# Kernel tuning notes

Hardware: AMD Instinct MI355X
Metric: run time of the kernel (lower is better)

The kernel has to match this reference:

```python
import jax, jax.numpy as jnp
import numpy as np

B = 512        # batch size
NCLASS = 128   # number of classes == embedding dim (per module docstring)
K = 8          # topk hard mining
MARGIN = 1.0
P = 1.0 / NCLASS  # default p = 1/nclass


def _pairwise_distances(x):
    # Euclidean distance matrix, with the zero-distance sqrt-safety trick
    dot = x @ x.T                      # (B, B)
    sq = jnp.diag(dot)                 # (B,)
    d = sq[None, :] - 2.0 * dot + sq[:, None]
    d = jnp.maximum(d, 0.0)
    zmask = (d == 0.0).astype(x.dtype)
    return (1.0 - zmask) * jnp.sqrt(d + zmask * 1e-16)


def _topk_rows_mask(valid):
    # torch .topk(k, dim=0, largest=True) + scatter_(0, idx, True):
    # per column, mark the k rows with the largest values.
    _, idx = jax.lax.top_k(valid.T, K)                 # (B, K): row indices per column
    mT = jnp.zeros((B, B), dtype=bool).at[jnp.arange(B)[:, None], idx].set(True)
    return mT.T                                        # back to (row, col) layout


def _forward(x, target):
    d = _pairwise_distances(x)                         # (B, B)
    sim = target[None, :] == target[:, None]           # (B, B) same-class mask

    # hard positives: largest same-class distances per column
    hard_pos = _topk_rows_mask(jnp.where(sim, d, -jnp.inf)) & sim
    # hard negatives: smallest different-class distances per column
    hard_neg = _topk_rows_mask(-jnp.where(sim, jnp.inf, d)) & (~sim)

    # minor-class anchors: class count < int(p * batch)
    boundary = int(P * B)
    cnt = jnp.zeros((NCLASS,), dtype=jnp.int32).at[target].add(1)
    anchors = cnt[target] < boundary                   # (B,)

    eye = jnp.eye(B, dtype=bool)
    mask_ap = (~eye) & anchors[:, None] & hard_pos     # (B, B)
    mask_an = anchors[:, None] & hard_neg              # (B, B)

    # O(B^3) triplet tensor
    t = d[:, :, None] - d[:, None, :] + MARGIN         # (B, B, B)
    m = mask_ap[:, :, None] & mask_an[:, None, :]
    t = jnp.maximum(m.astype(x.dtype) * t, 0.0)
    num_pos = jnp.sum(t > 1e-7).astype(x.dtype)
    return jnp.sum(t) / (num_pos + 1e-7)


def setup_inputs() -> dict:
    key = jax.random.key(0)
    k1, k2 = jax.random.split(key)
    x = jax.random.normal(k1, (B, NCLASS), dtype=jnp.float32)
    target = jax.random.randint(k2, (B,), 0, NCLASS)
    return {"x": x, "target": target}


def reference(x, target):
    return _forward(x, target)
```

## Files before the change

kernel.cpp:

```cpp
#include <hip/hip_runtime.h>
#include <math.h>

#define BB 512
#define DD 128
#define KK 8
#define BOUNDARY 4


__global__ __launch_bounds__(256) void fused_kernel(
    const float* __restrict__ x, const int* __restrict__ tgt,
    float* __restrict__ partS, int* __restrict__ partC)
{
    __shared__ float4 xi4[DD / 4];
    __shared__ float s_vn[BB];
    __shared__ float s_sq[BB];
    __shared__ int   s_tgt[BB];
    __shared__ int   s_cnt[128];
    __shared__ int   s_sel[KK];
    __shared__ int   s_pr[16], s_pj[16];
    __shared__ int   s_np;

    int k = blockIdx.x;
    int t = threadIdx.x;
    if (t < DD / 4) xi4[t] = ((const float4*)(x + k * DD))[t];
    if (t < 128) s_cnt[t] = 0;
    if (t == 0) s_np = 0;
    s_tgt[t]       = tgt[t];
    s_tgt[t + 256] = tgt[t + 256];
    __syncthreads();
    int tk = s_tgt[k];

    float q0 = 0.f, q1 = 0.f, q2 = 0.f, q3 = 0.f;
    for (int c = 0; c < DD / 4; ++c) {
        float4 a = xi4[c];
        q0 += a.x * a.x; q1 += a.y * a.y; q2 += a.z * a.z; q3 += a.w * a.w;
    }
    float sqk = (q0 + q1) + (q2 + q3);

    {
        int g = t >> 3, sub = t & 7;
        for (int pass = 0; pass < 16; ++pass) {
            int r = pass * 32 + g;
            const float4* xr = (const float4*)(x + r * DD);
            float d0 = 0.f, d1 = 0.f, d2 = 0.f, d3 = 0.f;
            float s0 = 0.f, s1 = 0.f, s2 = 0.f, s3 = 0.f;
            {
                float4 a = xi4[sub],      b = xr[sub];
                d0 = a.x*b.x + a.y*b.y + a.z*b.z + a.w*b.w;
                s0 = b.x*b.x + b.y*b.y + b.z*b.z + b.w*b.w;
            }
            {
                float4 a = xi4[sub + 8],  b = xr[sub + 8];
                d1 = a.x*b.x + a.y*b.y + a.z*b.z + a.w*b.w;
                s1 = b.x*b.x + b.y*b.y + b.z*b.z + b.w*b.w;
            }
            {
                float4 a = xi4[sub + 16], b = xr[sub + 16];
                d2 = a.x*b.x + a.y*b.y + a.z*b.z + a.w*b.w;
                s2 = b.x*b.x + b.y*b.y + b.z*b.z + b.w*b.w;
            }
            {
                float4 a = xi4[sub + 24], b = xr[sub + 24];
                d3 = a.x*b.x + a.y*b.y + a.z*b.z + a.w*b.w;
                s3 = b.x*b.x + b.y*b.y + b.z*b.z + b.w*b.w;
            }
            float dot = (d0 + d1) + (d2 + d3);
            float sq  = (s0 + s1) + (s2 + s3);
            for (int off = 4; off > 0; off >>= 1) {
                dot += __shfl_down(dot, off, 8);
                sq  += __shfl_down(sq,  off, 8);
            }
            if (sub == 0) {
                float dsq = fmaxf((sqk + sq) - 2.f * dot, 0.f);
                float dv = (dsq == 0.f) ? 0.f : sqrtf(dsq);
                s_sq[r] = sq;
                s_vn[r] = (s_tgt[r] == tk) ? -INFINITY : -dv;
            }
        }
    }
    __syncthreads();

    int wave = t >> 6, lane = t & 63;
    if (wave == 0) {
        float v[8];
        for (int q = 0; q < 8; ++q) v[q] = s_vn[q * 64 + lane];
        for (int pass = 0; pass < KK; ++pass) {
            float bv = -INFINITY; int bq = -1;
            for (int q = 0; q < 8; ++q)
                if (v[q] > bv) { bv = v[q]; bq = q; }
            int bi = (bq >= 0) ? (bq * 64 + lane) : (1 << 30);
            for (int off = 32; off > 0; off >>= 1) {
                float ov = __shfl_down(bv, off);
                int   oi = __shfl_down(bi, off);
                if (ov > bv || (ov == bv && oi < bi)) { bv = ov; bi = oi; }
            }
            bv = __shfl(bv, 0); bi = __shfl(bi, 0);
            if (lane == 0) s_sel[pass] = (bv == -INFINITY) ? -1 : bi;
            if ((bi & 63) == lane) v[bi >> 6] = -INFINITY;
        }
    } else if (wave == 1) {
        for (int q = 0; q < 8; ++q) atomicAdd(&s_cnt[s_tgt[q * 64 + lane]], 1);
    }
    __syncthreads();

    {
        int p = t >> 5, l = t & 31;
        int r = s_sel[p];
        if (r >= 0) {
            int tr = s_tgt[r];
            if (s_cnt[tr] < BOUNDARY) {
                for (int j = l; j < BB; j += 32)
                    if (j != r && s_tgt[j] == tr) {
                        int idx = atomicAdd(&s_np, 1);
                        s_pr[idx] = r; s_pj[idx] = j;
                    }
            }
        }
    }
    __syncthreads();

    float s = 0.f; int c = 0;
    if (t < s_np) {
        int r = s_pr[t], j = s_pj[t];
        const float4* xr = (const float4*)(x + r * DD);
        const float4* xj = (const float4*)(x + j * DD);
        float d0 = 0.f, d1 = 0.f, d2 = 0.f, d3 = 0.f;
        for (int cc = 0; cc < DD / 4; ++cc) {
            float4 a = xr[cc], b = xj[cc];
            d0 += a.x * b.x; d1 += a.y * b.y; d2 += a.z * b.z; d3 += a.w * b.w;
        }
        float dot = (d0 + d1) + (d2 + d3);
        float dsq = fmaxf((s_sq[r] + s_sq[j]) - 2.f * dot, 0.f);
        float dpos = (dsq == 0.f) ? 0.f : sqrtf(dsq);
        float tv = dpos + s_vn[r] + 1.0f;
        if (tv > 0.f) { s = tv; c = (tv > 1e-7f) ? 1 : 0; }
    }
    if (wave == 0) {
        for (int off = 32; off > 0; off >>= 1) {
            s += __shfl_down(s, off);
            c += __shfl_down(c, off);
        }
        if (lane == 0) { partS[k] = s; partC[k] = c; }
    }
}

__global__ __launch_bounds__(64) void fin_kernel(
    const float* __restrict__ partS, const int* __restrict__ partC,
    float* __restrict__ out)
{
    int lane = threadIdx.x;
    const float4* pS = (const float4*)partS;
    const int4*   pC = (const int4*)partC;
    float4 a = pS[lane], b = pS[lane + 64];
    int4   u = pC[lane], v = pC[lane + 64];
    float S = ((a.x + a.y) + (a.z + a.w)) + ((b.x + b.y) + (b.z + b.w));
    int   C = ((u.x + u.y) + (u.z + u.w)) + ((v.x + v.y) + (v.z + v.w));
    for (int off = 32; off > 0; off >>= 1) {
        S += __shfl_down(S, off);
        C += __shfl_down(C, off);
    }
    if (lane == 0) out[0] = S / ((float)C + 1e-7f);
}

extern "C" void kernel_launch(void* const* d_in, const int* in_sizes, int n_in,
                              void* d_out, int out_size, void* d_ws, size_t ws_size,
                              hipStream_t stream) {
    const float* x   = (const float*)d_in[0];
    const int*   tgt = (const int*)d_in[1];
    float* out = (float*)d_out;

    char* ws = (char*)d_ws;
    float* partS = (float*)(ws + 0);
    int*   partC = (int*)(ws + 2048);

    fused_kernel<<<BB, 256, 0, stream>>>(x, tgt, partS, partC);
    fin_kernel<<<1, 64, 0, stream>>>(partS, partC, out);
}
```

Before: 73.94 us.

## Process two anchor columns per block to reuse row loads

Each block now handles two columns (k and k+256), so every row of x loaded from global memory is dotted against two anchor vectors, and the per-block setup (target load, class counting) is shared. The grid is halved to 256 blocks, with two waves running top-k in parallel and the pair buffer doubled to hold both columns' candidates. The aim is to halve redundant global row reads and fixed per-block overhead, at the cost of fewer blocks (less parallelism across CUs) and more registers and shared memory per block.

```diff
diff --git a/kernel.cpp b/kernel.cpp
--- a/kernel.cpp
+++ b/kernel.cpp
@@ -5,85 +5,108 @@
 #define DD 128
 #define KK 8
 #define BOUNDARY 4
+#define NBLK 256
 
 
 __global__ __launch_bounds__(256) void fused_kernel(
     const float* __restrict__ x, const int* __restrict__ tgt,
     float* __restrict__ partS, int* __restrict__ partC)
 {
-    __shared__ float4 xi4[DD / 4];
-    __shared__ float s_vn[BB];
+    __shared__ float4 xiA[DD / 4];
+    __shared__ float4 xiB[DD / 4];
+    __shared__ float s_vnA[BB];
+    __shared__ float s_vnB[BB];
     __shared__ float s_sq[BB];
     __shared__ int   s_tgt[BB];
     __shared__ int   s_cnt[128];
-    __shared__ int   s_sel[KK];
-    __shared__ int   s_pr[16], s_pj[16];
+    __shared__ int   s_selA[KK];
+    __shared__ int   s_selB[KK];
+    __shared__ int   s_pr[32], s_pj[32];
+    __shared__ float s_pd[32];
     __shared__ int   s_np;
 
-    int k = blockIdx.x;
+    int kA = blockIdx.x;
+    int kB = blockIdx.x + NBLK;
     int t = threadIdx.x;
-    if (t < DD / 4) xi4[t] = ((const float4*)(x + k * DD))[t];
+    if (t < DD / 4) {
+        xiA[t] = ((const float4*)(x + kA * DD))[t];
+        xiB[t] = ((const float4*)(x + kB * DD))[t];
+    }
     if (t < 128) s_cnt[t] = 0;
     if (t == 0) s_np = 0;
     s_tgt[t]       = tgt[t];
     s_tgt[t + 256] = tgt[t + 256];
     __syncthreads();
-    int tk = s_tgt[k];
-
-    float q0 = 0.f, q1 = 0.f, q2 = 0.f, q3 = 0.f;
+    int tkA = s_tgt[kA];
+    int tkB = s_tgt[kB];
+
+    float a0 = 0.f, a1 = 0.f, a2 = 0.f, a3 = 0.f;
+    float b0 = 0.f, b1 = 0.f, b2 = 0.f, b3 = 0.f;
     for (int c = 0; c < DD / 4; ++c) {
-        float4 a = xi4[c];
-        q0 += a.x * a.x; q1 += a.y * a.y; q2 += a.z * a.z; q3 += a.w * a.w;
-    }
-    float sqk = (q0 + q1) + (q2 + q3);
+        float4 a = xiA[c], b = xiB[c];
+        a0 += a.x * a.x; a1 += a.y * a.y; a2 += a.z * a.z; a3 += a.w * a.w;
+        b0 += b.x * b.x; b1 += b.y * b.y; b2 += b.z * b.z; b3 += b.w * b.w;
+    }
+    float sqkA = (a0 + a1) + (a2 + a3);
+    float sqkB = (b0 + b1) + (b2 + b3);
 
     {
         int g = t >> 3, sub = t & 7;
         for (int pass = 0; pass < 16; ++pass) {
             int r = pass * 32 + g;
             const float4* xr = (const float4*)(x + r * DD);
-            float d0 = 0.f, d1 = 0.f, d2 = 0.f, d3 = 0.f;
-            float s0 = 0.f, s1 = 0.f, s2 = 0.f, s3 = 0.f;
-            {
-                float4 a = xi4[sub],      b = xr[sub];
-                d0 = a.x*b.x + a.y*b.y + a.z*b.z + a.w*b.w;
-                s0 = b.x*b.x + b.y*b.y + b.z*b.z + b.w*b.w;
-            }
-            {
-                float4 a = xi4[sub + 8],  b = xr[sub + 8];
-                d1 = a.x*b.x + a.y*b.y + a.z*b.z + a.w*b.w;
-                s1 = b.x*b.x + b.y*b.y + b.z*b.z + b.w*b.w;
-            }
-            {
-                float4 a = xi4[sub + 16], b = xr[sub + 16];
-                d2 = a.x*b.x + a.y*b.y + a.z*b.z + a.w*b.w;
-                s2 = b.x*b.x + b.y*b.y + b.z*b.z + b.w*b.w;
-            }
-            {
-                float4 a = xi4[sub + 24], b = xr[sub + 24];
-                d3 = a.x*b.x + a.y*b.y + a.z*b.z + a.w*b.w;
-                s3 = b.x*b.x + b.y*b.y + b.z*b.z + b.w*b.w;
-            }
-            float dot = (d0 + d1) + (d2 + d3);
-            float sq  = (s0 + s1) + (s2 + s3);
+            float dA0, dA1, dA2, dA3, dB0, dB1, dB2, dB3, s0, s1, s2, s3;
+            {
+                float4 a = xiA[sub],      p = xiB[sub],      b = xr[sub];
+                dA0 = a.x*b.x + a.y*b.y + a.z*b.z + a.w*b.w;
+                dB0 = p.x*b.x + p.y*b.y + p.z*b.z + p.w*b.w;
+                s0  = b.x*b.x + b.y*b.y + b.z*b.z + b.w*b.w;
+            }
+            {
+                float4 a = xiA[sub + 8],  p = xiB[sub + 8],  b = xr[sub + 8];
+                dA1 = a.x*b.x + a.y*b.y + a.z*b.z + a.w*b.w;
+                dB1 = p.x*b.x + p.y*b.y + p.z*b.z + p.w*b.w;
+                s1  = b.x*b.x + b.y*b.y + b.z*b.z + b.w*b.w;
+            }
+            {
+                float4 a = xiA[sub + 16], p = xiB[sub + 16], b = xr[sub + 16];
+                dA2 = a.x*b.x + a.y*b.y + a.z*b.z + a.w*b.w;
+                dB2 = p.x*b.x + p.y*b.y + p.z*b.z + p.w*b.w;
+                s2  = b.x*b.x + b.y*b.y + b.z*b.z + b.w*b.w;
+            }
+            {
+                float4 a = xiA[sub + 24], p = xiB[sub + 24], b = xr[sub + 24];
+                dA3 = a.x*b.x + a.y*b.y + a.z*b.z + a.w*b.w;
+                dB3 = p.x*b.x + p.y*b.y + p.z*b.z + p.w*b.w;
+                s3  = b.x*b.x + b.y*b.y + b.z*b.z + b.w*b.w;
+            }
+            float dotA = (dA0 + dA1) + (dA2 + dA3);
+            float dotB = (dB0 + dB1) + (dB2 + dB3);
+            float sq   = (s0 + s1) + (s2 + s3);
             for (int off = 4; off > 0; off >>= 1) {
-                dot += __shfl_down(dot, off, 8);
-                sq  += __shfl_down(sq,  off, 8);
+                dotA += __shfl_down(dotA, off, 8);
+                dotB += __shfl_down(dotB, off, 8);
+                sq   += __shfl_down(sq,   off, 8);
             }
             if (sub == 0) {
-                float dsq = fmaxf((sqk + sq) - 2.f * dot, 0.f);
-                float dv = (dsq == 0.f) ? 0.f : sqrtf(dsq);
-                s_sq[r] = sq;
-                s_vn[r] = (s_tgt[r] == tk) ? -INFINITY : -dv;
+                float dsqA = fmaxf((sqkA + sq) - 2.f * dotA, 0.f);
+                float dsqB = fmaxf((sqkB + sq) - 2.f * dotB, 0.f);
+                float dvA = (dsqA == 0.f) ? 0.f : sqrtf(dsqA);
+                float dvB = (dsqB == 0.f) ? 0.f : sqrtf(dsqB);
+                s_sq[r]  = sq;
+                s_vnA[r] = (s_tgt[r] == tkA) ? -INFINITY : -dvA;
+                s_vnB[r] = (s_tgt[r] == tkB) ? -INFINITY : -dvB;
             }
         }
     }
     __syncthreads();
 
     int wave = t >> 6, lane = t & 63;
-    if (wave == 0) {
+    if (wave == 0 || wave == 1) {
+        const float* vn = (wave == 0) ? s_vnA : s_vnB;
+        int*        sel = (wave == 0) ? s_selA : s_selB;
         float v[8];
-        for (int q = 0; q < 8; ++q) v[q] = s_vn[q * 64 + lane];
+        for (int q = 0; q < 8; ++q) v[q] = vn[q * 64 + lane];
         for (int pass = 0; pass < KK; ++pass) {
             float bv = -INFINITY; int bq = -1;
             for (int q = 0; q < 8; ++q)
@@ -95,24 +118,26 @@
                 if (ov > bv || (ov == bv && oi < bi)) { bv = ov; bi = oi; }
             }
             bv = __shfl(bv, 0); bi = __shfl(bi, 0);
-            if (lane == 0) s_sel[pass] = (bv == -INFINITY) ? -1 : bi;
+            if (lane == 0) sel[pass] = (bv == -INFINITY) ? -1 : bi;
             if ((bi & 63) == lane) v[bi >> 6] = -INFINITY;
         }
-    } else if (wave == 1) {
+    } else if (wave == 2) {
         for (int q = 0; q < 8; ++q) atomicAdd(&s_cnt[s_tgt[q * 64 + lane]], 1);
     }
     __syncthreads();
 
     {
-        int p = t >> 5, l = t & 31;
-        int r = s_sel[p];
+        int p = t >> 4, l = t & 15;
+        int col = p >> 3, slot = p & 7;
+        int r = col ? s_selB[slot] : s_selA[slot];
         if (r >= 0) {
             int tr = s_tgt[r];
             if (s_cnt[tr] < BOUNDARY) {
-                for (int j = l; j < BB; j += 32)
+                float vn = col ? s_vnB[r] : s_vnA[r];
+                for (int j = l; j < BB; j += 16)
                     if (j != r && s_tgt[j] == tr) {
                         int idx = atomicAdd(&s_np, 1);
-                        s_pr[idx] = r; s_pj[idx] = j;
+                        s_pr[idx] = r; s_pj[idx] = j; s_pd[idx] = vn;
                     }
             }
         }
@@ -132,7 +157,7 @@
         float dot = (d0 + d1) + (d2 + d3);
         float dsq = fmaxf((s_sq[r] + s_sq[j]) - 2.f * dot, 0.f);
         float dpos = (dsq == 0.f) ? 0.f : sqrtf(dsq);
-        float tv = dpos + s_vn[r] + 1.0f;
+        float tv = dpos + s_pd[t] + 1.0f;
         if (tv > 0.f) { s = tv; c = (tv > 1e-7f) ? 1 : 0; }
     }
     if (wave == 0) {
@@ -140,7 +165,7 @@
             s += __shfl_down(s, off);
             c += __shfl_down(c, off);
         }
-        if (lane == 0) { partS[k] = s; partC[k] = c; }
+        if (lane == 0) { partS[blockIdx.x] = s; partC[blockIdx.x] = c; }
     }
 }
 
@@ -151,10 +176,10 @@
     int lane = threadIdx.x;
     const float4* pS = (const float4*)partS;
     const int4*   pC = (const int4*)partC;
-    float4 a = pS[lane], b = pS[lane + 64];
-    int4   u = pC[lane], v = pC[lane + 64];
-    float S = ((a.x + a.y) + (a.z + a.w)) + ((b.x + b.y) + (b.z + b.w));
-    int   C = ((u.x + u.y) + (u.z + u.w)) + ((v.x + v.y) + (v.z + v.w));
+    float4 a = pS[lane];
+    int4   u = pC[lane];
+    float S = (a.x + a.y) + (a.z + a.w);
+    int   C = (u.x + u.y) + (u.z + u.w);
     for (int off = 32; off > 0; off >>= 1) {
         S += __shfl_down(S, off);
         C += __shfl_down(C, off);
@@ -171,8 +196,8 @@
 
     char* ws = (char*)d_ws;
     float* partS = (float*)(ws + 0);
-    int*   partC = (int*)(ws + 2048);
-
-    fused_kernel<<<BB, 256, 0, stream>>>(x, tgt, partS, partC);
+    int*   partC = (int*)(ws + 1024);
+
+    fused_kernel<<<NBLK, 256, 0, stream>>>(x, tgt, partS, partC);
     fin_kernel<<<1, 64, 0, stream>>>(partS, partC, out);
 }
```

Result: slower. 77.37 us (+4.6%).
